# Performance work log

Hardware: AMD Instinct MI355X
Metric: run time of the kernel (lower is better)

## Reference

```python
import jax, jax.numpy as jnp
import numpy as np

B, N, DIM, H = 8, 2048, 64, 8  # per-head dim == DIM (module convention: inner_dim = dim * n_heads)


def setup_inputs() -> dict:
    key = jax.random.key(0)
    k1, k2, k3 = jax.random.split(key, 3)
    x = jax.random.normal(k1, (B, N, DIM), dtype=jnp.float32)
    W_qkv = jax.random.normal(k2, (DIM, 3 * H * DIM), dtype=jnp.float32) * (DIM ** -0.5)
    W_out = jax.random.normal(k3, (H * DIM, DIM), dtype=jnp.float32) * ((H * DIM) ** -0.5)
    b_out = jnp.zeros((DIM,), dtype=jnp.float32)
    return {"x": x, "W_qkv": W_qkv, "W_out": W_out, "b_out": b_out}


def reference(x, W_qkv, W_out, b_out):
    b, n, d = x.shape
    h = W_qkv.shape[1] // (3 * d)
    qkv = x @ W_qkv                                   # [b, n, 3*h*d]
    q, k, v = jnp.split(qkv, 3, axis=-1)              # each [b, n, h*d]
    def to_heads(t):
        return t.reshape(b, n, h, d).transpose(0, 2, 1, 3)  # [b, h, n, d]
    q, k, v = map(to_heads, (q, k, v))
    scale = d ** -0.5
    dot = jnp.einsum('bhid,bhjd->bhij', q, k) * scale  # [b, h, n, n]
    A = jax.nn.softmax(dot, axis=-1)
    z = jnp.einsum('bhij,bhjd->bhid', A, v)            # [b, h, n, d]
    z = z.transpose(0, 2, 1, 3).reshape(b, n, h * d)   # [b, n, h*d]
    return z @ W_out + b_out                           # [b, n, d]
```

## Files before the change

### kernel.cpp

```cpp
#include <hip/hip_runtime.h>
#include <math.h>

#define BB 8
#define NN 2048
#define DD 64
#define HH 8
#define BH (BB*HH)
#define HD (HH*DD)
#define NROWS (BB*NN)
#define QKV_COLS (3*HD)

typedef __bf16 bf16_8 __attribute__((ext_vector_type(8)));
typedef __bf16 bf16_4 __attribute__((ext_vector_type(4)));
typedef float  f32_16 __attribute__((ext_vector_type(16)));
typedef float  f32_4  __attribute__((ext_vector_type(4)));
typedef int    i32_2  __attribute__((ext_vector_type(2)));

__device__ __forceinline__ unsigned pack_bf16(float a, float b) {
  union { __bf16 h[2]; unsigned u; } t;
  t.h[0] = (__bf16)a; t.h[1] = (__bf16)b;
  return t.u;
}

__device__ __forceinline__ float fast_exp2(float x) {
#if __has_builtin(__builtin_amdgcn_exp2f)
  return __builtin_amdgcn_exp2f(x);
#else
  return __expf(x * 0.69314718056f);
#endif
}

__global__ __launch_bounds__(256) void wtrans_kernel(
    const float* __restrict__ Wqkv, const float* __restrict__ Wout,
    __bf16* __restrict__ Wtq, __bf16* __restrict__ Wto) {
  int idx = blockIdx.x * 256 + threadIdx.x;
  if (idx < 64 * QKV_COLS) {
    int k = idx / QKV_COLS, col = idx % QKV_COLS;
    float v = Wqkv[idx];
    if (col < HD) v *= 0.125f * 1.44269504088896f;
    Wtq[col * 64 + k] = (__bf16)v;
    (void)k;
  } else {
    int j = idx - 64 * QKV_COLS;
    int k = j >> 6, col = j & 63;
    Wto[col * 512 + k] = (__bf16)Wout[j];
  }
}

__global__ __launch_bounds__(256) void qkv_kernel(
    const float* __restrict__ x, const __bf16* __restrict__ Wtq,
    __bf16* __restrict__ Q, __bf16* __restrict__ K, __bf16* __restrict__ Vt) {
  __shared__ __bf16 T[4][64][34];
  const int lane = threadIdx.x & 63;
  const int wave = threadIdx.x >> 6;
  const int l31  = lane & 31, lhi = lane >> 5;
  const int cg   = blockIdx.x;
  const int row0 = blockIdx.y * 128 + wave * 32;

  const float* xr = x + (size_t)(row0 + l31) * 64 + lhi * 8;
  bf16_8 af[4];
#pragma unroll
  for (int s = 0; s < 4; s++) {
    f32_4 a0 = *(const f32_4*)(xr + s * 16);
    f32_4 a1 = *(const f32_4*)(xr + s * 16 + 4);
#pragma unroll
    for (int j = 0; j < 4; j++) { af[s][j] = (__bf16)a0[j]; af[s][4 + j] = (__bf16)a1[j]; }
  }

  f32_16 C0, C1;
#pragma unroll
  for (int i = 0; i < 16; i++) { C0[i] = 0.f; C1[i] = 0.f; }

  const __bf16* wb = Wtq + (size_t)cg * 64 * 64 + lhi * 8;
#pragma unroll
  for (int s = 0; s < 4; s++) {
    bf16_8 b0 = *(const bf16_8*)(wb + (size_t)l31 * 64 + s * 16);
    bf16_8 b1 = *(const bf16_8*)(wb + (size_t)(32 + l31) * 64 + s * 16);
    C0 = __builtin_amdgcn_mfma_f32_32x32x16_bf16(af[s], b0, C0, 0, 0, 0);
    C1 = __builtin_amdgcn_mfma_f32_32x32x16_bf16(af[s], b1, C1, 0, 0, 0);
  }

  const int col0  = cg * 64;
  const int which = col0 >> 9;
  const int h     = (col0 >> 6) & 7;
  const int b     = row0 >> 11;
  const int n0l   = row0 & 2047;

  if (which < 2) {
    __bf16* dst = (which == 0) ? Q : K;
#pragma unroll
    for (int r = 0; r < 16; r++) {
      int nl = (r & 3) + 8 * (r >> 2) + 4 * lhi;
      size_t base = (((size_t)(b * HH + h) * NN) + n0l + nl) * DD;
      dst[base + l31]      = (__bf16)C0[r];
      dst[base + 32 + l31] = (__bf16)C1[r];
    }
  } else {
    __bf16 (*Tw)[34] = T[wave];
#pragma unroll
    for (int r = 0; r < 16; r++) {
      int nl = (r & 3) + 8 * (r >> 2) + 4 * lhi;
      Tw[l31][nl]      = (__bf16)C0[r];
      Tw[32 + l31][nl] = (__bf16)C1[r];
    }
    __bf16* dst = Vt + (((size_t)(b * HH + h) * DD) + lane) * NN + n0l;
#pragma unroll
    for (int j = 0; j < 4; j++) {
      *(bf16_8*)(dst + j * 8) = *(const bf16_8*)(&Tw[lane][j * 8]);
    }
  }
}

__global__ __launch_bounds__(256, 3) void attn_kernel(
    const __bf16* __restrict__ Q, const __bf16* __restrict__ K,
    const __bf16* __restrict__ Vt, __bf16* __restrict__ z) {
  __shared__ __bf16 Ks[128 * 72];
  __shared__ __bf16 Vs[64 * 136];

  const int tid  = threadIdx.x;
  const int wave = tid >> 6;
  const int lane = tid & 63;
  const int l31  = lane & 31;
  const int lhi  = lane >> 5;
  const int xl   = lane ^ 32;
  const int bh   = blockIdx.x >> 4;
  const int q0   = (blockIdx.x & 15) * 128 + wave * 32;

  const __bf16* Qbase = Q + ((size_t)bh * NN + q0 + l31) * DD + lhi * 8;
  bf16_8 qf[4];
#pragma unroll
  for (int s = 0; s < 4; s++) qf[s] = *(const bf16_8*)(Qbase + s * 16);

  f32_16 O0, O1;
#pragma unroll
  for (int i = 0; i < 16; i++) { O0[i] = 0.f; O1[i] = 0.f; }
  float ls0 = 0.f, ls1 = 0.f;

  const __bf16* Kb = K  + (size_t)bh * NN * DD;
  const __bf16* Vb = Vt + (size_t)bh * DD * NN;

  const int krow = tid >> 3, kcol = (tid & 7) * 8;
  const int vrow = tid >> 4, vcol = (tid & 15) * 8;
  const __bf16* kgl = Kb + krow * 64 + kcol;
  const __bf16* vgl = Vb + (size_t)vrow * NN + vcol;
  __bf16* klds = &Ks[krow * 72 + kcol];
  __bf16* vlds = &Vs[vrow * 136 + vcol];

  bf16_8 gk[4], gv[4];
#pragma unroll
  for (int i = 0; i < 4; i++) {
    gk[i] = *(const bf16_8*)(kgl + i * 32 * 64);
    gv[i] = *(const bf16_8*)(vgl + i * 16 * NN);
  }

  for (int kt = 0; kt < NN; kt += 128) {
    __syncthreads();
#pragma unroll
    for (int i = 0; i < 4; i++) {
      *(bf16_8*)(klds + i * 32 * 72)  = gk[i];
      *(bf16_8*)(vlds + i * 16 * 136) = gv[i];
    }
    __syncthreads();
    if (kt + 128 < NN) {
#pragma unroll
      for (int i = 0; i < 4; i++) {
        gk[i] = *(const bf16_8*)(kgl + (kt + 128) * 64 + i * 32 * 64);
        gv[i] = *(const bf16_8*)(vgl + (kt + 128) + i * 16 * NN);
      }
    }

#pragma unroll
    for (int hf = 0; hf < 2; hf++) {
      f32_16 S0, S1;
#pragma unroll
      for (int i = 0; i < 16; i++) { S0[i] = 0.f; S1[i] = 0.f; }
#pragma unroll
      for (int s = 0; s < 4; s++) {
        bf16_8 kb0 = *(const bf16_8*)(&Ks[(hf * 64 + l31) * 72 + s * 16 + lhi * 8]);
        bf16_8 kb1 = *(const bf16_8*)(&Ks[(hf * 64 + 32 + l31) * 72 + s * 16 + lhi * 8]);
        S0 = __builtin_amdgcn_mfma_f32_32x32x16_bf16(kb0, qf[s], S0, 0, 0, 0);
        S1 = __builtin_amdgcn_mfma_f32_32x32x16_bf16(kb1, qf[s], S1, 0, 0, 0);
      }

      unsigned pk[16];
#pragma unroll
      for (int t = 0; t < 8; t++) {
        float a = fast_exp2(S0[2 * t]), b = fast_exp2(S0[2 * t + 1]);
        float c = fast_exp2(S1[2 * t]), d = fast_exp2(S1[2 * t + 1]);
        ls0 += a + b;
        ls1 += c + d;
        pk[t]     = pack_bf16(a, b);
        pk[8 + t] = pack_bf16(c, d);
      }

#pragma unroll
      for (int g = 0; g < 4; g++) {
        const int base = (g >> 1) * 8 + (g & 1) * 4;
        int a0 = (int)pk[base + 0], a1 = (int)pk[base + 1];
        int a2 = (int)pk[base + 2], a3 = (int)pk[base + 3];
        union { unsigned u[4]; bf16_8 v; } F;
#if __has_builtin(__builtin_amdgcn_permlane32_swap)
        i32_2 r02 = __builtin_amdgcn_permlane32_swap(a0, a2, false, false);
        i32_2 r13 = __builtin_amdgcn_permlane32_swap(a1, a3, false, false);
        F.u[0] = (unsigned)r02.x; F.u[2] = (unsigned)r02.y;
        F.u[1] = (unsigned)r13.x; F.u[3] = (unsigned)r13.y;
#else
        unsigned w0 = (unsigned)__shfl(a0, xl, 64);
        unsigned w1 = (unsigned)__shfl(a1, xl, 64);
        unsigned w2 = (unsigned)__shfl(a2, xl, 64);
        unsigned w3 = (unsigned)__shfl(a3, xl, 64);
        F.u[0] = lhi ? w2 : (unsigned)a0;
        F.u[1] = lhi ? w3 : (unsigned)a1;
        F.u[2] = lhi ? (unsigned)a2 : w0;
        F.u[3] = lhi ? (unsigned)a3 : w1;
#endif
        bf16_8 va0 = *(const bf16_8*)(&Vs[l31 * 136 + hf * 64 + g * 16 + lhi * 8]);
        bf16_8 va1 = *(const bf16_8*)(&Vs[(32 + l31) * 136 + hf * 64 + g * 16 + lhi * 8]);
        O0 = __builtin_amdgcn_mfma_f32_32x32x16_bf16(va0, F.v, O0, 0, 0, 0);
        O1 = __builtin_amdgcn_mfma_f32_32x32x16_bf16(va1, F.v, O1, 0, 0, 0);
      }
    }
  }

  float lsum = ls0 + ls1;
  lsum += __shfl_xor(lsum, 32, 64);
  const float inv = 1.f / lsum;

  __syncthreads();
  __bf16* ow = Ks + wave * (32 * 72);
#pragma unroll
  for (int g = 0; g < 4; g++) {
    bf16_4 p0, p1;
#pragma unroll
    for (int i = 0; i < 4; i++) {
      p0[i] = (__bf16)(O0[4 * g + i] * inv);
      p1[i] = (__bf16)(O1[4 * g + i] * inv);
    }
    const int d0 = 8 * g + 4 * lhi;
    *(bf16_4*)(ow + l31 * 72 + d0)      = p0;
    *(bf16_4*)(ow + l31 * 72 + 32 + d0) = p1;
  }
  const int b = bh >> 3, h = bh & 7;
  const int qr = lane >> 1, c0 = (lane & 1) * 32;
  __bf16* zp = z + ((size_t)b * NN + q0 + qr) * HD + h * DD + c0;
#pragma unroll
  for (int j = 0; j < 4; j++) {
    *(bf16_8*)(zp + 8 * j) = *(const bf16_8*)(ow + qr * 72 + c0 + 8 * j);
  }
}

__global__ __launch_bounds__(256) void out_proj_kernel(
    const __bf16* __restrict__ z, const __bf16* __restrict__ Wto,
    const float* __restrict__ bout, float* __restrict__ out) {
  __shared__ float red[2][64][36];
  const int tid  = threadIdx.x;
  const int wave = tid >> 6, lane = tid & 63;
  const int rt   = wave >> 1, kh = wave & 1;
  const int l31  = lane & 31, lhi = lane >> 5;
  const int row0 = blockIdx.x * 64 + rt * 32;

  const __bf16* zr = z   + (size_t)(row0 + l31) * HD + kh * 256 + lhi * 8;
  const __bf16* w0 = Wto + (size_t)l31 * HD        + kh * 256 + lhi * 8;
  const __bf16* w1 = Wto + (size_t)(32 + l31) * HD + kh * 256 + lhi * 8;

  f32_16 C0, C1;
#pragma unroll
  for (int i = 0; i < 16; i++) { C0[i] = 0.f; C1[i] = 0.f; }

#pragma unroll
  for (int s = 0; s < 16; s++) {
    bf16_8 a  = *(const bf16_8*)(zr + s * 16);
    bf16_8 b0 = *(const bf16_8*)(w0 + s * 16);
    bf16_8 b1 = *(const bf16_8*)(w1 + s * 16);
    C0 = __builtin_amdgcn_mfma_f32_32x32x16_bf16(a, b0, C0, 0, 0, 0);
    C1 = __builtin_amdgcn_mfma_f32_32x32x16_bf16(a, b1, C1, 0, 0, 0);
  }

  float* rw = &red[rt][lane][0];
  if (kh) {
#pragma unroll
    for (int r = 0; r < 16; r++) { rw[r] = C0[r]; rw[16 + r] = C1[r]; }
  }
  __syncthreads();
  if (!kh) {
    const float bi0 = bout[l31], bi1 = bout[32 + l31];
#pragma unroll
    for (int r = 0; r < 16; r++) {
      int n = row0 + (r & 3) + 8 * (r >> 2) + 4 * lhi;
      out[(size_t)n * 64 + l31]      = C0[r] + rw[r]      + bi0;
      out[(size_t)n * 64 + 32 + l31] = C1[r] + rw[16 + r] + bi1;
    }
  }
}

extern "C" void kernel_launch(void* const* d_in, const int* in_sizes, int n_in,
                              void* d_out, int out_size, void* d_ws, size_t ws_size,
                              hipStream_t stream) {
  const float* x    = (const float*)d_in[0];
  const float* Wqkv = (const float*)d_in[1];
  const float* Wout = (const float*)d_in[2];
  const float* bout = (const float*)d_in[3];
  float* out = (float*)d_out;

  const size_t buf_elems = (size_t)BB * HH * NN * DD;
  __bf16* Qw  = (__bf16*)d_ws;
  __bf16* Kw  = Qw  + buf_elems;
  __bf16* Vtw = Kw  + buf_elems;
  __bf16* zw  = Vtw + buf_elems;
  __bf16* Wtq = zw  + buf_elems;
  __bf16* Wto = Wtq + (size_t)QKV_COLS * 64;

  wtrans_kernel<<<512, 256, 0, stream>>>(Wqkv, Wout, Wtq, Wto);
  qkv_kernel<<<dim3(QKV_COLS / 64, NROWS / 128), 256, 0, stream>>>(x, Wtq, Qw, Kw, Vtw);
  attn_kernel<<<BH * (NN / 128), 256, 0, stream>>>(Qw, Kw, Vtw, zw);
  out_proj_kernel<<<NROWS / 64, 256, 0, stream>>>(zw, Wto, bout, out);
}
```

Baseline: 192.9 us.

## Fuse output projection into attention kernel and drop LDS staging of K/V

The output projection is folded into the attention kernel epilogue: each head's normalized output is multiplied by its slice of W_out, which is pre-swizzled into MFMA operand layout. The partial results are summed across heads with float atomicAdd into a zeroed output. This removes the z intermediate buffer and the separate out_proj launch. K and V tiles are now read directly from global memory into registers per 64-key chunk instead of being staged through shared memory with barriers. The trade-offs are atomic contention (8 heads per output element), nondeterministic summation order, and loss of K/V sharing across the four waves, which raises L2 traffic.

After: 343.0 us. +77.9%, slower.

```diff
diff --git a/kernel.cpp b/kernel.cpp
--- a/kernel.cpp
+++ b/kernel.cpp
@@ -11,7 +11,6 @@
 #define QKV_COLS (3*HD)
 
 typedef __bf16 bf16_8 __attribute__((ext_vector_type(8)));
-typedef __bf16 bf16_4 __attribute__((ext_vector_type(4)));
 typedef float  f32_16 __attribute__((ext_vector_type(16)));
 typedef float  f32_4  __attribute__((ext_vector_type(4)));
 typedef int    i32_2  __attribute__((ext_vector_type(2)));
@@ -32,18 +31,23 @@
 
 __global__ __launch_bounds__(256) void wtrans_kernel(
     const float* __restrict__ Wqkv, const float* __restrict__ Wout,
-    __bf16* __restrict__ Wtq, __bf16* __restrict__ Wto) {
+    __bf16* __restrict__ Wtq, __bf16* __restrict__ Wob) {
   int idx = blockIdx.x * 256 + threadIdx.x;
   if (idx < 64 * QKV_COLS) {
-    int k = idx / QKV_COLS, col = idx % QKV_COLS;
+    int col = idx % QKV_COLS;
+    int k   = idx / QKV_COLS;
     float v = Wqkv[idx];
     if (col < HD) v *= 0.125f * 1.44269504088896f;
     Wtq[col * 64 + k] = (__bf16)v;
-    (void)k;
   } else {
-    int j = idx - 64 * QKV_COLS;
-    int k = j >> 6, col = j & 63;
-    Wto[col * 512 + k] = (__bf16)Wout[j];
+    int j2 = idx - 64 * QKV_COLS;
+    int dfull = j2 >> 6, co = j2 & 63;
+    int h  = dfull >> 6, dl = dfull & 63;
+    int s  = dl >> 4, rem = dl & 15;
+    int lh = rem >> 3, jj = rem & 7;
+    int t  = co >> 5, lc = co & 31;
+    int lane = lh * 32 + lc;
+    Wob[(((h * 8 + t * 4 + s) * 64) + lane) * 8 + jj] = (__bf16)Wout[j2];
   }
 }
 
@@ -113,10 +117,8 @@
 
 __global__ __launch_bounds__(256, 3) void attn_kernel(
     const __bf16* __restrict__ Q, const __bf16* __restrict__ K,
-    const __bf16* __restrict__ Vt, __bf16* __restrict__ z) {
-  __shared__ __bf16 Ks[128 * 72];
-  __shared__ __bf16 Vs[64 * 136];
-
+    const __bf16* __restrict__ Vt, const __bf16* __restrict__ Wob,
+    const float* __restrict__ bout, float* __restrict__ out) {
   const int tid  = threadIdx.x;
   const int wave = tid >> 6;
   const int lane = tid & 63;
@@ -139,86 +141,65 @@
   const __bf16* Kb = K  + (size_t)bh * NN * DD;
   const __bf16* Vb = Vt + (size_t)bh * DD * NN;
 
-  const int krow = tid >> 3, kcol = (tid & 7) * 8;
-  const int vrow = tid >> 4, vcol = (tid & 15) * 8;
-  const __bf16* kgl = Kb + krow * 64 + kcol;
-  const __bf16* vgl = Vb + (size_t)vrow * NN + vcol;
-  __bf16* klds = &Ks[krow * 72 + kcol];
-  __bf16* vlds = &Vs[vrow * 136 + vcol];
-
-  bf16_8 gk[4], gv[4];
-#pragma unroll
-  for (int i = 0; i < 4; i++) {
-    gk[i] = *(const bf16_8*)(kgl + i * 32 * 64);
-    gv[i] = *(const bf16_8*)(vgl + i * 16 * NN);
-  }
-
-  for (int kt = 0; kt < NN; kt += 128) {
-    __syncthreads();
-#pragma unroll
-    for (int i = 0; i < 4; i++) {
-      *(bf16_8*)(klds + i * 32 * 72)  = gk[i];
-      *(bf16_8*)(vlds + i * 16 * 136) = gv[i];
-    }
-    __syncthreads();
-    if (kt + 128 < NN) {
-#pragma unroll
-      for (int i = 0; i < 4; i++) {
-        gk[i] = *(const bf16_8*)(kgl + (kt + 128) * 64 + i * 32 * 64);
-        gv[i] = *(const bf16_8*)(vgl + (kt + 128) + i * 16 * NN);
-      }
-    }
-
-#pragma unroll
-    for (int hf = 0; hf < 2; hf++) {
-      f32_16 S0, S1;
-#pragma unroll
-      for (int i = 0; i < 16; i++) { S0[i] = 0.f; S1[i] = 0.f; }
-#pragma unroll
-      for (int s = 0; s < 4; s++) {
-        bf16_8 kb0 = *(const bf16_8*)(&Ks[(hf * 64 + l31) * 72 + s * 16 + lhi * 8]);
-        bf16_8 kb1 = *(const bf16_8*)(&Ks[(hf * 64 + 32 + l31) * 72 + s * 16 + lhi * 8]);
-        S0 = __builtin_amdgcn_mfma_f32_32x32x16_bf16(kb0, qf[s], S0, 0, 0, 0);
-        S1 = __builtin_amdgcn_mfma_f32_32x32x16_bf16(kb1, qf[s], S1, 0, 0, 0);
-      }
-
-      unsigned pk[16];
-#pragma unroll
-      for (int t = 0; t < 8; t++) {
-        float a = fast_exp2(S0[2 * t]), b = fast_exp2(S0[2 * t + 1]);
-        float c = fast_exp2(S1[2 * t]), d = fast_exp2(S1[2 * t + 1]);
-        ls0 += a + b;
-        ls1 += c + d;
-        pk[t]     = pack_bf16(a, b);
-        pk[8 + t] = pack_bf16(c, d);
-      }
-
-#pragma unroll
-      for (int g = 0; g < 4; g++) {
-        const int base = (g >> 1) * 8 + (g & 1) * 4;
-        int a0 = (int)pk[base + 0], a1 = (int)pk[base + 1];
-        int a2 = (int)pk[base + 2], a3 = (int)pk[base + 3];
-        union { unsigned u[4]; bf16_8 v; } F;
+  for (int c = 0; c < 32; c++) {
+    const __bf16* kf = Kb + (size_t)(c * 64 + l31) * 64 + lhi * 8;
+    const __bf16* vf = Vb + (size_t)l31 * NN + c * 64 + lhi * 8;
+
+    bf16_8 kb0[4], kb1[4], va0[4], va1[4];
+#pragma unroll
+    for (int s = 0; s < 4; s++) {
+      kb0[s] = *(const bf16_8*)(kf + s * 16);
+      kb1[s] = *(const bf16_8*)(kf + 32 * 64 + s * 16);
+    }
+#pragma unroll
+    for (int g = 0; g < 4; g++) {
+      va0[g] = *(const bf16_8*)(vf + g * 16);
+      va1[g] = *(const bf16_8*)(vf + (size_t)32 * NN + g * 16);
+    }
+
+    f32_16 S0, S1;
+#pragma unroll
+    for (int i = 0; i < 16; i++) { S0[i] = 0.f; S1[i] = 0.f; }
+#pragma unroll
+    for (int s = 0; s < 4; s++) {
+      S0 = __builtin_amdgcn_mfma_f32_32x32x16_bf16(kb0[s], qf[s], S0, 0, 0, 0);
+      S1 = __builtin_amdgcn_mfma_f32_32x32x16_bf16(kb1[s], qf[s], S1, 0, 0, 0);
+    }
+
+    unsigned pk[16];
+#pragma unroll
+    for (int t = 0; t < 8; t++) {
+      float a = fast_exp2(S0[2 * t]), b = fast_exp2(S0[2 * t + 1]);
+      float cc = fast_exp2(S1[2 * t]), d = fast_exp2(S1[2 * t + 1]);
+      ls0 += a + b;
+      ls1 += cc + d;
+      pk[t]     = pack_bf16(a, b);
+      pk[8 + t] = pack_bf16(cc, d);
+    }
+
+#pragma unroll
+    for (int g = 0; g < 4; g++) {
+      const int base = (g >> 1) * 8 + (g & 1) * 4;
+      int a0 = (int)pk[base + 0], a1 = (int)pk[base + 1];
+      int a2 = (int)pk[base + 2], a3 = (int)pk[base + 3];
+      union { unsigned u[4]; bf16_8 v; } F;
 #if __has_builtin(__builtin_amdgcn_permlane32_swap)
-        i32_2 r02 = __builtin_amdgcn_permlane32_swap(a0, a2, false, false);
-        i32_2 r13 = __builtin_amdgcn_permlane32_swap(a1, a3, false, false);
-        F.u[0] = (unsigned)r02.x; F.u[2] = (unsigned)r02.y;
-        F.u[1] = (unsigned)r13.x; F.u[3] = (unsigned)r13.y;
+      i32_2 r02 = __builtin_amdgcn_permlane32_swap(a0, a2, false, false);
+      i32_2 r13 = __builtin_amdgcn_permlane32_swap(a1, a3, false, false);
+      F.u[0] = (unsigned)r02.x; F.u[2] = (unsigned)r02.y;
+      F.u[1] = (unsigned)r13.x; F.u[3] = (unsigned)r13.y;
 #else
-        unsigned w0 = (unsigned)__shfl(a0, xl, 64);
-        unsigned w1 = (unsigned)__shfl(a1, xl, 64);
-        unsigned w2 = (unsigned)__shfl(a2, xl, 64);
-        unsigned w3 = (unsigned)__shfl(a3, xl, 64);
-        F.u[0] = lhi ? w2 : (unsigned)a0;
-        F.u[1] = lhi ? w3 : (unsigned)a1;
-        F.u[2] = lhi ? (unsigned)a2 : w0;
-        F.u[3] = lhi ? (unsigned)a3 : w1;
+      unsigned w0 = (unsigned)__shfl(a0, xl, 64);
+      unsigned w1 = (unsigned)__shfl(a1, xl, 64);
+      unsigned w2 = (unsigned)__shfl(a2, xl, 64);
+      unsigned w3 = (unsigned)__shfl(a3, xl, 64);
+      F.u[0] = lhi ? w2 : (unsigned)a0;
+      F.u[1] = lhi ? w3 : (unsigned)a1;
+      F.u[2] = lhi ? (unsigned)a2 : w0;
+      F.u[3] = lhi ? (unsigned)a3 : w1;
 #endif
-        bf16_8 va0 = *(const bf16_8*)(&Vs[l31 * 136 + hf * 64 + g * 16 + lhi * 8]);
-        bf16_8 va1 = *(const bf16_8*)(&Vs[(32 + l31) * 136 + hf * 64 + g * 16 + lhi * 8]);
-        O0 = __builtin_amdgcn_mfma_f32_32x32x16_bf16(va0, F.v, O0, 0, 0, 0);
-        O1 = __builtin_amdgcn_mfma_f32_32x32x16_bf16(va1, F.v, O1, 0, 0, 0);
-      }
+      O0 = __builtin_amdgcn_mfma_f32_32x32x16_bf16(va0[g], F.v, O0, 0, 0, 0);
+      O1 = __builtin_amdgcn_mfma_f32_32x32x16_bf16(va1[g], F.v, O1, 0, 0, 0);
     }
   }
 
@@ -226,70 +207,55 @@
   lsum += __shfl_xor(lsum, 32, 64);
   const float inv = 1.f / lsum;
 
-  __syncthreads();
-  __bf16* ow = Ks + wave * (32 * 72);
-#pragma unroll
-  for (int g = 0; g < 4; g++) {
-    bf16_4 p0, p1;
-#pragma unroll
-    for (int i = 0; i < 4; i++) {
-      p0[i] = (__bf16)(O0[4 * g + i] * inv);
-      p1[i] = (__bf16)(O1[4 * g + i] * inv);
-    }
-    const int d0 = 8 * g + 4 * lhi;
-    *(bf16_4*)(ow + l31 * 72 + d0)      = p0;
-    *(bf16_4*)(ow + l31 * 72 + 32 + d0) = p1;
-  }
-  const int b = bh >> 3, h = bh & 7;
-  const int qr = lane >> 1, c0 = (lane & 1) * 32;
-  __bf16* zp = z + ((size_t)b * NN + q0 + qr) * HD + h * DD + c0;
-#pragma unroll
-  for (int j = 0; j < 4; j++) {
-    *(bf16_8*)(zp + 8 * j) = *(const bf16_8*)(ow + qr * 72 + c0 + 8 * j);
-  }
-}
-
-__global__ __launch_bounds__(256) void out_proj_kernel(
-    const __bf16* __restrict__ z, const __bf16* __restrict__ Wto,
-    const float* __restrict__ bout, float* __restrict__ out) {
-  __shared__ float red[2][64][36];
-  const int tid  = threadIdx.x;
-  const int wave = tid >> 6, lane = tid & 63;
-  const int rt   = wave >> 1, kh = wave & 1;
-  const int l31  = lane & 31, lhi = lane >> 5;
-  const int row0 = blockIdx.x * 64 + rt * 32;
-
-  const __bf16* zr = z   + (size_t)(row0 + l31) * HD + kh * 256 + lhi * 8;
-  const __bf16* w0 = Wto + (size_t)l31 * HD        + kh * 256 + lhi * 8;
-  const __bf16* w1 = Wto + (size_t)(32 + l31) * HD + kh * 256 + lhi * 8;
-
-  f32_16 C0, C1;
-#pragma unroll
-  for (int i = 0; i < 16; i++) { C0[i] = 0.f; C1[i] = 0.f; }
-
-#pragma unroll
-  for (int s = 0; s < 16; s++) {
-    bf16_8 a  = *(const bf16_8*)(zr + s * 16);
-    bf16_8 b0 = *(const bf16_8*)(w0 + s * 16);
-    bf16_8 b1 = *(const bf16_8*)(w1 + s * 16);
-    C0 = __builtin_amdgcn_mfma_f32_32x32x16_bf16(a, b0, C0, 0, 0, 0);
-    C1 = __builtin_amdgcn_mfma_f32_32x32x16_bf16(a, b1, C1, 0, 0, 0);
-  }
-
-  float* rw = &red[rt][lane][0];
-  if (kh) {
-#pragma unroll
-    for (int r = 0; r < 16; r++) { rw[r] = C0[r]; rw[16 + r] = C1[r]; }
-  }
-  __syncthreads();
-  if (!kh) {
-    const float bi0 = bout[l31], bi1 = bout[32 + l31];
-#pragma unroll
-    for (int r = 0; r < 16; r++) {
-      int n = row0 + (r & 3) + 8 * (r >> 2) + 4 * lhi;
-      out[(size_t)n * 64 + l31]      = C0[r] + rw[r]      + bi0;
-      out[(size_t)n * 64 + 32 + l31] = C1[r] + rw[16 + r] + bi1;
-    }
+  unsigned ok[16];
+#pragma unroll
+  for (int t = 0; t < 8; t++) {
+    ok[t]     = pack_bf16(O0[2 * t] * inv, O0[2 * t + 1] * inv);
+    ok[8 + t] = pack_bf16(O1[2 * t] * inv, O1[2 * t + 1] * inv);
+  }
+
+  const int h = bh & 7;
+  const __bf16* Wbh = Wob + (size_t)h * 8 * 64 * 8;
+  f32_16 D0, D1;
+#pragma unroll
+  for (int i = 0; i < 16; i++) { D0[i] = 0.f; D1[i] = 0.f; }
+
+#pragma unroll
+  for (int s = 0; s < 4; s++) {
+    const int base = (s >> 1) * 8 + (s & 1) * 4;
+    int a0 = (int)ok[base + 0], a1 = (int)ok[base + 1];
+    int a2 = (int)ok[base + 2], a3 = (int)ok[base + 3];
+    union { unsigned u[4]; bf16_8 v; } F;
+#if __has_builtin(__builtin_amdgcn_permlane32_swap)
+    i32_2 r02 = __builtin_amdgcn_permlane32_swap(a0, a2, false, false);
+    i32_2 r13 = __builtin_amdgcn_permlane32_swap(a1, a3, false, false);
+    F.u[0] = (unsigned)r02.x; F.u[2] = (unsigned)r02.y;
+    F.u[1] = (unsigned)r13.x; F.u[3] = (unsigned)r13.y;
+#else
+    unsigned w0 = (unsigned)__shfl(a0, xl, 64);
+    unsigned w1 = (unsigned)__shfl(a1, xl, 64);
+    unsigned w2 = (unsigned)__shfl(a2, xl, 64);
+    unsigned w3 = (unsigned)__shfl(a3, xl, 64);
+    F.u[0] = lhi ? w2 : (unsigned)a0;
+    F.u[1] = lhi ? w3 : (unsigned)a1;
+    F.u[2] = lhi ? (unsigned)a2 : w0;
+    F.u[3] = lhi ? (unsigned)a3 : w1;
+#endif
+    bf16_8 b0 = *(const bf16_8*)(Wbh + ((size_t)(0 * 4 + s) * 64 + lane) * 8);
+    bf16_8 b1 = *(const bf16_8*)(Wbh + ((size_t)(1 * 4 + s) * 64 + lane) * 8);
+    D0 = __builtin_amdgcn_mfma_f32_32x32x16_bf16(F.v, b0, D0, 0, 0, 0);
+    D1 = __builtin_amdgcn_mfma_f32_32x32x16_bf16(F.v, b1, D1, 0, 0, 0);
+  }
+
+  const int b = bh >> 3;
+  const float bi0 = (h == 0) ? bout[l31]      : 0.f;
+  const float bi1 = (h == 0) ? bout[32 + l31] : 0.f;
+  float* ob = out + ((size_t)b * NN + q0) * 64;
+#pragma unroll
+  for (int r = 0; r < 16; r++) {
+    int qr = (r & 3) + 8 * (r >> 2) + 4 * lhi;
+    atomicAdd(&ob[(size_t)qr * 64 + l31],      D0[r] + bi0);
+    atomicAdd(&ob[(size_t)qr * 64 + 32 + l31], D1[r] + bi1);
   }
 }
 
@@ -306,12 +272,11 @@
   __bf16* Qw  = (__bf16*)d_ws;
   __bf16* Kw  = Qw  + buf_elems;
   __bf16* Vtw = Kw  + buf_elems;
-  __bf16* zw  = Vtw + buf_elems;
-  __bf16* Wtq = zw  + buf_elems;
-  __bf16* Wto = Wtq + (size_t)QKV_COLS * 64;
-
-  wtrans_kernel<<<512, 256, 0, stream>>>(Wqkv, Wout, Wtq, Wto);
+  __bf16* Wtq = Vtw + buf_elems;
+  __bf16* Wob = Wtq + (size_t)QKV_COLS * 64;
+
+  hipMemsetAsync(out, 0, (size_t)NROWS * DD * sizeof(float), stream);
+  wtrans_kernel<<<512, 256, 0, stream>>>(Wqkv, Wout, Wtq, Wob);
   qkv_kernel<<<dim3(QKV_COLS / 64, NROWS / 128), 256, 0, stream>>>(x, Wtq, Qw, Kw, Vtw);
-  attn_kernel<<<BH * (NN / 128), 256, 0, stream>>>(Qw, Kw, Vtw, zw);
-  out_proj_kernel<<<NROWS / 64, 256, 0, stream>>>(zw, Wto, bout, out);
-}
+  attn_kernel<<<BH * (NN / 128), 256, 0, stream>>>(Qw, Kw, Vtw, Wob, bout, out);
+}
```
